# Kernel tuning notes

Hardware: AMD Instinct MI355X
Metric: run time of the kernel (lower is better)

The kernel has to match this reference:

```python
import jax, jax.numpy as jnp
import numpy as np

D_MODEL = 1024
N_HEADS = 16
D_HEAD = D_MODEL // N_HEADS

def setup_inputs() -> dict:
    key = jax.random.key(0)
    ks = jax.random.split(key, 5)
    B, T = 4, 2048
    s = 1.0 / np.sqrt(D_MODEL)
    return {
        "x": jax.random.normal(ks[0], (B, T, D_MODEL), dtype=jnp.float32),
        "qkv_w": jax.random.normal(ks[1], (3 * D_MODEL, D_MODEL), dtype=jnp.float32) * s,
        "qkv_b": jnp.zeros((3 * D_MODEL,), dtype=jnp.float32),
        "out_w": jax.random.normal(ks[2], (D_MODEL, D_MODEL), dtype=jnp.float32) * s,
        "out_b": jnp.zeros((D_MODEL,), dtype=jnp.float32),
    }

def reference(x, qkv_w, qkv_b, out_w, out_b):
    B, T, D = x.shape
    # fused QKV projection: [B,T,3D] -> [3,B,H,T,dh]
    qkv = (x @ qkv_w.T + qkv_b).reshape(B, T, 3, N_HEADS, D_HEAD)
    qkv = jnp.transpose(qkv, (2, 0, 3, 1, 4))
    q, k, v = qkv[0], qkv[1], qkv[2]
    scale = 1.0 / np.sqrt(D_HEAD).astype(np.float32)
    scores = jnp.einsum("bhqd,bhkd->bhqk", q, k) * scale
    attn = jax.nn.softmax(scores, axis=-1)
    ctx = jnp.einsum("bhqk,bhkd->bhqd", attn, v)  # [B,H,T,dh]
    ctx = jnp.transpose(ctx, (0, 2, 1, 3)).reshape(B, T, D)
    return ctx @ out_w.T + out_b
```

## Files before the change

### kernel.cpp

```cpp
#include <hip/hip_runtime.h>
#include <hip/hip_bf16.h>
#include <cstdint>
#include <cstddef>


#define SEQ 2048
#define DM 1024

typedef __attribute__((ext_vector_type(8))) short bf16x8;
typedef __attribute__((ext_vector_type(4))) short bf16x4;
typedef __attribute__((ext_vector_type(4))) float f32x4;

static __device__ __forceinline__ short f2bf(float f) {
  union { float f; uint32_t u; } v; v.f = f;
  uint32_t r = v.u + 0x7fffu + ((v.u >> 16) & 1u);
  return (short)(r >> 16);
}

typedef const __attribute__((address_space(1))) unsigned int* gas_ptr;
typedef __attribute__((address_space(3))) unsigned int* las_ptr;
static __device__ __forceinline__ void gl2lds16(const void* g, void* l) {
  __builtin_amdgcn_global_load_lds((gas_ptr)g, (las_ptr)l, 16, 0, 0);
}

static __device__ __forceinline__ unsigned permhi(float a_odd, float a_even) {
  union { float f; unsigned u; } x, y; x.f = a_odd; y.f = a_even;
  return __builtin_amdgcn_perm(x.u, y.u, 0x07060302u);
}
static __device__ __forceinline__ bf16x8 pack8t(const float* e) {
  union { bf16x8 v; unsigned u[4]; } r;
  r.u[0] = permhi(e[1], e[0]);
  r.u[1] = permhi(e[3], e[2]);
  r.u[2] = permhi(e[5], e[4]);
  r.u[3] = permhi(e[7], e[6]);
  return r.v;
}

static __device__ __forceinline__ int swz(int r) {
  return (r & 3) | (((r >> 3) & 1) << 2);
}

__global__ __launch_bounds__(256)
void cvt_bf16(const float* __restrict__ src, short* __restrict__ dst) {
  int i = blockIdx.x * 256 + threadIdx.x;
  float4 v = ((const float4*)src)[i];
  bf16x4 p = { f2bf(v.x), f2bf(v.y), f2bf(v.z), f2bf(v.w) };
  ((bf16x4*)dst)[i] = p;
}

__global__ __launch_bounds__(256, 2)
void qkv_gemm(const short* __restrict__ Xb, const short* __restrict__ Wb,
              const float* __restrict__ bias,
              short* __restrict__ Q, short* __restrict__ K,
              short* __restrict__ Vt) {
  __shared__ short As[2][128 * 64];
  __shared__ short Bs[2][128 * 64];
  const int tid  = threadIdx.x;
  const int m0   = blockIdx.x * 128;
  const int n0   = blockIdx.y * 128;
  const int lane = tid & 63;
  const int w    = tid >> 6;
  const int wm   = (w >> 1) * 64, wn = (w & 1) * 64;
  const int l15  = lane & 15, quad = lane >> 4;

  int g_row[4], g_col[4];
#pragma unroll
  for (int p = 0; p < 4; p++) {
    int r = p * 32 + w * 8 + (lane >> 3);
    g_row[p] = r;
    g_col[p] = ((lane & 7) ^ swz(r)) << 3;
  }
  int aoff[4][2], boff[4][2];
#pragma unroll
  for (int i = 0; i < 4; i++)
#pragma unroll
    for (int ks = 0; ks < 2; ks++) {
      int Ra = wm + i * 16 + l15;
      aoff[i][ks] = Ra * 128 + (((ks * 4 + quad) ^ swz(Ra)) << 4);
      int Rb = wn + i * 16 + l15;
      boff[i][ks] = Rb * 128 + (((ks * 4 + quad) ^ swz(Rb)) << 4);
    }

  f32x4 acc[4][4];
  for (int i = 0; i < 4; i++)
    for (int j = 0; j < 4; j++) acc[i][j] = (f32x4)0.0f;

#pragma unroll
  for (int p = 0; p < 4; p++) {
    gl2lds16(&Xb[(size_t)(m0 + g_row[p]) * DM + g_col[p]], &As[0][(p * 32 + w * 8) * 64]);
    gl2lds16(&Wb[(size_t)(n0 + g_row[p]) * DM + g_col[p]], &Bs[0][(p * 32 + w * 8) * 64]);
  }

  for (int t = 0; t < 16; t++) {
    const int cur = t & 1;
    if (t + 1 < 16) {
      const int kk = (t + 1) * 64;
#pragma unroll
      for (int p = 0; p < 4; p++) {
        gl2lds16(&Xb[(size_t)(m0 + g_row[p]) * DM + kk + g_col[p]], &As[cur ^ 1][(p * 32 + w * 8) * 64]);
        gl2lds16(&Wb[(size_t)(n0 + g_row[p]) * DM + kk + g_col[p]], &Bs[cur ^ 1][(p * 32 + w * 8) * 64]);
      }
      asm volatile("s_waitcnt vmcnt(8)" ::: "memory");
    } else {
      asm volatile("s_waitcnt vmcnt(0)" ::: "memory");
    }
    __builtin_amdgcn_s_barrier();
    __builtin_amdgcn_sched_barrier(0);

    const char* Ab = (const char*)&As[cur][0];
    const char* Bb = (const char*)&Bs[cur][0];
#pragma unroll
    for (int ks = 0; ks < 2; ks++) {
      bf16x8 af[4], bfr[4];
      for (int i = 0; i < 4; i++) af[i]  = *(const bf16x8*)(Ab + aoff[i][ks]);
      for (int j = 0; j < 4; j++) bfr[j] = *(const bf16x8*)(Bb + boff[j][ks]);
      for (int i = 0; i < 4; i++)
        for (int j = 0; j < 4; j++)
          acc[i][j] = __builtin_amdgcn_mfma_f32_16x16x32_bf16(af[i], bfr[j], acc[i][j], 0, 0, 0);
    }
    __builtin_amdgcn_sched_barrier(0);
    __builtin_amdgcn_s_barrier();
    __builtin_amdgcn_sched_barrier(0);
  }

  const float C1 = 0.18033688011112042f;
  const int qkv = n0 >> 10;
  for (int i = 0; i < 4; i++) {
    const int m = m0 + wm + i * 16 + quad * 4;
    const int bb = m >> 11, t = m & 2047;
    for (int j = 0; j < 4; j++) {
      const int f  = n0 + wn + j * 16 + l15;
      const int fi = f & 1023;
      const int h  = fi >> 6, d = fi & 63;
      const float bv = bias[f];
      if (qkv == 2) {
        bf16x4 pk = { f2bf(acc[i][j][0] + bv), f2bf(acc[i][j][1] + bv),
                      f2bf(acc[i][j][2] + bv), f2bf(acc[i][j][3] + bv) };
        *(bf16x4*)&Vt[((size_t)(bb * 16 + h) * 64 + d) * SEQ + t] = pk;
      } else {
        short* dst = (qkv == 0) ? Q : K;
        const float sc = (qkv == 0) ? C1 : 1.0f;
        size_t base = ((size_t)(bb * 16 + h) * SEQ + t) * 64 + d;
        for (int r = 0; r < 4; r++)
          dst[base + (size_t)r * 64] = f2bf((acc[i][j][r] + bv) * sc);
      }
    }
  }
}

__global__ __launch_bounds__(256, 4)
void attn(const short* __restrict__ Q, const short* __restrict__ K,
          const short* __restrict__ Vt, short* __restrict__ ctx) {
  __shared__ short Ks[2][64 * 64];
  __shared__ short Vs[2][64 * 64];
  const int tid  = threadIdx.x;
  const int w    = tid >> 6, lane = tid & 63;
  const int l15  = lane & 15, quad = lane >> 4;
  const int bh   = blockIdx.y;
  const int qr   = blockIdx.x * 128 + w * 32;
  const short* Kb = &K[(size_t)bh * SEQ * 64];
  const short* Vb = &Vt[(size_t)bh * 64 * SEQ];

  const int kperm = (l15 >> 2) * 8 + (l15 & 3);

  int dr[2], dc[2];
#pragma unroll
  for (int p = 0; p < 2; p++) {
    int ci = p * 256 + w * 64 + lane;
    dr[p] = ci >> 3;
    dc[p] = (ci & 7) ^ swz(ci >> 3);
  }
  const short* kp[2];
  const short* vp[2];
#pragma unroll
  for (int p = 0; p < 2; p++) {
    kp[p] = &Kb[(size_t)(64 + dr[p]) * 64 + dc[p] * 8];
    vp[p] = &Vb[(size_t)dr[p] * SEQ + 64 + dc[p] * 8];
  }

  int koff[2][2][2][2];
  int voff[2][4][2];
#pragma unroll
  for (int blk = 0; blk < 2; blk++)
#pragma unroll
    for (int tau = 0; tau < 2; tau++)
#pragma unroll
      for (int ks = 0; ks < 2; ks++) {
        int R = blk * 32 + kperm + tau * 4;
        int c = (ks * 4 + quad) ^ swz(R);
        int off = (R * 8 + c) * 16;
        koff[0][blk][tau][ks] = off;
        koff[1][blk][tau][ks] = off + 8192;
      }
#pragma unroll
  for (int dt = 0; dt < 4; dt++)
#pragma unroll
    for (int blk = 0; blk < 2; blk++) {
      int R = dt * 16 + l15;
      int c = (blk * 4 + quad) ^ swz(R);
      int off = (R * 8 + c) * 16;
      voff[0][dt][blk] = off;
      voff[1][dt][blk] = off + 8192;
    }
  const char* KsB = (const char*)&Ks[0][0];
  const char* VsB = (const char*)&Vs[0][0];

  bf16x8 qf[2][2];
#pragma unroll
  for (int mt = 0; mt < 2; mt++)
#pragma unroll
    for (int ks = 0; ks < 2; ks++)
      qf[mt][ks] = *(const bf16x8*)&Q[(size_t)bh * SEQ * 64 + (size_t)(qr + mt * 16 + l15) * 64 + ks * 32 + quad * 8];

  f32x4 O[2][4];
#pragma unroll
  for (int mt = 0; mt < 2; mt++)
    for (int dt = 0; dt < 4; dt++) O[mt][dt] = (f32x4)0.0f;
  f32x4 psA[2];
  psA[0] = (f32x4)0.0f; psA[1] = (f32x4)0.0f;
  const short one_bf = (short)0x3F80;
  const bf16x8 ones = { one_bf, one_bf, one_bf, one_bf, one_bf, one_bf, one_bf, one_bf };

#pragma unroll
  for (int p = 0; p < 2; p++) {
    gl2lds16(&Kb[(size_t)dr[p] * 64 + dc[p] * 8],  &Ks[0][(p * 256 + w * 64) * 8]);
    gl2lds16(&Vb[(size_t)dr[p] * SEQ + dc[p] * 8], &Vs[0][(p * 256 + w * 64) * 8]);
  }
  __syncthreads();

  for (int k0 = 0; k0 < SEQ; k0 += 128) {
#pragma unroll
    for (int half = 0; half < 2; half++) {
      const bool doPf = (half == 0) || (k0 + 128 < SEQ);
      if (doPf) {
#pragma unroll
        for (int p = 0; p < 2; p++) {
          gl2lds16(kp[p], &Ks[half ^ 1][(p * 256 + w * 64) * 8]);
          gl2lds16(vp[p], &Vs[half ^ 1][(p * 256 + w * 64) * 8]);
        }
      }
#pragma unroll
      for (int p = 0; p < 2; p++) { kp[p] += 64 * 64; vp[p] += 64; }

      bf16x8 kf[2][2][2];
#pragma unroll
      for (int blk = 0; blk < 2; blk++)
#pragma unroll
        for (int tau = 0; tau < 2; tau++)
#pragma unroll
          for (int ks = 0; ks < 2; ks++)
            kf[blk][tau][ks] = *(const bf16x8*)(KsB + koff[half][blk][tau][ks]);

      f32x4 S[2][2][2];
#pragma unroll
      for (int mt = 0; mt < 2; mt++)
#pragma unroll
        for (int blk = 0; blk < 2; blk++) {
          f32x4 S0 = (f32x4)0.0f, S1 = (f32x4)0.0f;
#pragma unroll
          for (int ks = 0; ks < 2; ks++) {
            S0 = __builtin_amdgcn_mfma_f32_16x16x32_bf16(kf[blk][0][ks], qf[mt][ks], S0, 0, 0, 0);
            S1 = __builtin_amdgcn_mfma_f32_16x16x32_bf16(kf[blk][1][ks], qf[mt][ks], S1, 0, 0, 0);
          }
          S[mt][blk][0] = S0; S[mt][blk][1] = S1;
        }

      bf16x8 vf[4][2];
#pragma unroll
      for (int dt = 0; dt < 4; dt++)
#pragma unroll
        for (int blk = 0; blk < 2; blk++)
          vf[dt][blk] = *(const bf16x8*)(VsB + voff[half][dt][blk]);

      bf16x8 pp[2][2];
#pragma unroll
      for (int mt = 0; mt < 2; mt++)
#pragma unroll
        for (int blk = 0; blk < 2; blk++) {
          float e[8];
#pragma unroll
          for (int r = 0; r < 4; r++) {
            e[r]     = exp2f(S[mt][blk][0][r]);
            e[4 + r] = exp2f(S[mt][blk][1][r]);
          }
          pp[mt][blk] = pack8t(e);
        }

#pragma unroll
      for (int blk = 0; blk < 2; blk++) {
#pragma unroll
        for (int dt = 0; dt < 4; dt++) {
          O[0][dt] = __builtin_amdgcn_mfma_f32_16x16x32_bf16(vf[dt][blk], pp[0][blk], O[0][dt], 0, 0, 0);
          O[1][dt] = __builtin_amdgcn_mfma_f32_16x16x32_bf16(vf[dt][blk], pp[1][blk], O[1][dt], 0, 0, 0);
        }
        psA[0] = __builtin_amdgcn_mfma_f32_16x16x32_bf16(ones, pp[0][blk], psA[0], 0, 0, 0);
        psA[1] = __builtin_amdgcn_mfma_f32_16x16x32_bf16(ones, pp[1][blk], psA[1], 0, 0, 0);
      }

      __syncthreads();
    }
  }

  const int bb = bh >> 4, h = bh & 15;
#pragma unroll
  for (int mt = 0; mt < 2; mt++) {
    float rinv = 1.0f / psA[mt][0];
    const int t = qr + mt * 16 + l15;
#pragma unroll
    for (int dt = 0; dt < 4; dt++) {
      bf16x4 ov = { f2bf(O[mt][dt][0] * rinv), f2bf(O[mt][dt][1] * rinv),
                    f2bf(O[mt][dt][2] * rinv), f2bf(O[mt][dt][3] * rinv) };
      *(bf16x4*)&ctx[(size_t)(bb * SEQ + t) * DM + h * 64 + dt * 16 + quad * 4] = ov;
    }
  }
}

__global__ __launch_bounds__(256, 2)
void out_gemm(const short* __restrict__ Cx, const short* __restrict__ Ob,
              const float* __restrict__ bias, float* __restrict__ Y) {
  __shared__ short As[2][128 * 64];
  __shared__ short Bs[2][128 * 64];
  const int tid  = threadIdx.x;
  const int m0   = blockIdx.x * 128;
  const int n0   = blockIdx.y * 128;
  const int lane = tid & 63;
  const int w    = tid >> 6;
  const int wm   = (w >> 1) * 64, wn = (w & 1) * 64;
  const int l15  = lane & 15, quad = lane >> 4;

  int g_row[4], g_col[4];
#pragma unroll
  for (int p = 0; p < 4; p++) {
    int r = p * 32 + w * 8 + (lane >> 3);
    g_row[p] = r;
    g_col[p] = ((lane & 7) ^ swz(r)) << 3;
  }
  int aoff[4][2], boff[4][2];
#pragma unroll
  for (int i = 0; i < 4; i++)
#pragma unroll
    for (int ks = 0; ks < 2; ks++) {
      int Ra = wm + i * 16 + l15;
      aoff[i][ks] = Ra * 128 + (((ks * 4 + quad) ^ swz(Ra)) << 4);
      int Rb = wn + i * 16 + l15;
      boff[i][ks] = Rb * 128 + (((ks * 4 + quad) ^ swz(Rb)) << 4);
    }

  f32x4 acc[4][4];
  for (int i = 0; i < 4; i++)
    for (int j = 0; j < 4; j++) acc[i][j] = (f32x4)0.0f;

#pragma unroll
  for (int p = 0; p < 4; p++) {
    gl2lds16(&Cx[(size_t)(m0 + g_row[p]) * DM + g_col[p]], &As[0][(p * 32 + w * 8) * 64]);
    gl2lds16(&Ob[(size_t)(n0 + g_row[p]) * DM + g_col[p]], &Bs[0][(p * 32 + w * 8) * 64]);
  }

  for (int t = 0; t < 16; t++) {
    const int cur = t & 1;
    if (t + 1 < 16) {
      const int kk = (t + 1) * 64;
#pragma unroll
      for (int p = 0; p < 4; p++) {
        gl2lds16(&Cx[(size_t)(m0 + g_row[p]) * DM + kk + g_col[p]], &As[cur ^ 1][(p * 32 + w * 8) * 64]);
        gl2lds16(&Ob[(size_t)(n0 + g_row[p]) * DM + kk + g_col[p]], &Bs[cur ^ 1][(p * 32 + w * 8) * 64]);
      }
      asm volatile("s_waitcnt vmcnt(8)" ::: "memory");
    } else {
      asm volatile("s_waitcnt vmcnt(0)" ::: "memory");
    }
    __builtin_amdgcn_s_barrier();
    __builtin_amdgcn_sched_barrier(0);

    const char* Ab = (const char*)&As[cur][0];
    const char* Bb = (const char*)&Bs[cur][0];
#pragma unroll
    for (int ks = 0; ks < 2; ks++) {
      bf16x8 af[4], bfr[4];
      for (int i = 0; i < 4; i++) af[i]  = *(const bf16x8*)(Ab + aoff[i][ks]);
      for (int j = 0; j < 4; j++) bfr[j] = *(const bf16x8*)(Bb + boff[j][ks]);
      for (int i = 0; i < 4; i++)
        for (int j = 0; j < 4; j++)
          acc[i][j] = __builtin_amdgcn_mfma_f32_16x16x32_bf16(af[i], bfr[j], acc[i][j], 0, 0, 0);
    }
    __builtin_amdgcn_sched_barrier(0);
    __builtin_amdgcn_s_barrier();
    __builtin_amdgcn_sched_barrier(0);
  }

  for (int i = 0; i < 4; i++) {
    const int m = m0 + wm + i * 16 + quad * 4;
    for (int j = 0; j < 4; j++) {
      const int n = n0 + wn + j * 16 + l15;
      const float bv = bias[n];
      for (int r = 0; r < 4; r++)
        Y[(size_t)(m + r) * DM + n] = acc[i][j][r] + bv;
    }
  }
}

extern "C" void kernel_launch(void* const* d_in, const int* in_sizes, int n_in,
                              void* d_out, int out_size, void* d_ws, size_t ws_size,
                              hipStream_t stream) {
  const float* x     = (const float*)d_in[0];
  const float* qkv_w = (const float*)d_in[1];
  const float* qkv_b = (const float*)d_in[2];
  const float* out_w = (const float*)d_in[3];
  const float* out_b = (const float*)d_in[4];
  float* out = (float*)d_out;

  const size_t NBH = (size_t)4 * 16 * SEQ * 64;
  short* Q   = (short*)d_ws;
  short* K   = Q + NBH;
  short* Vt  = K + NBH;
  short* ctx = Vt + NBH;
  short* Xb  = ctx;
  short* Ob  = Vt;
  short* Wb  = (short*)d_out;

  cvt_bf16<<<dim3(8192), 256, 0, stream>>>(x, Xb);
  cvt_bf16<<<dim3(3072), 256, 0, stream>>>(qkv_w, Wb);
  qkv_gemm<<<dim3(64, 24), 256, 0, stream>>>(Xb, Wb, qkv_b, Q, K, Vt);
  attn<<<dim3(SEQ / 128, 64), 256, 0, stream>>>(Q, K, Vt, ctx);
  cvt_bf16<<<dim3(1024), 256, 0, stream>>>(out_w, Ob);
  out_gemm<<<dim3(64, 8), 256, 0, stream>>>(ctx, Ob, out_b, out);
}
```

Before: 279.0 us.

## Enlarge QKV GEMM tile to 256x256 with 512 threads and fuse conversions

Grows the QKV projection GEMM block tile from 128x128 to 256x256 using 8 waves, each computing 128x64. This raises operand reuse from LDS and global memory. The main loop is restructured: it prefetches the next stage, hoists B fragments, wraps the MFMA block in s_setprio, and waits on vmcnt(0) before the barrier instead of a partial count. The two fp32-to-bf16 conversion launches for x and qkv_w are merged into one. The larger tile uses 128KB of LDS and many more accumulator registers, which lowers occupancy and leaves only 384 blocks.

```diff
diff --git a/kernel.cpp b/kernel.cpp
--- a/kernel.cpp
+++ b/kernel.cpp
@@ -48,48 +48,75 @@
   ((bf16x4*)dst)[i] = p;
 }
 
-__global__ __launch_bounds__(256, 2)
+__global__ __launch_bounds__(256)
+void cvt_bf16_2(const float* __restrict__ src1, short* __restrict__ dst1, int n1,
+                const float* __restrict__ src2, short* __restrict__ dst2) {
+  int b = blockIdx.x;
+  if (b < n1) {
+    int i = b * 256 + threadIdx.x;
+    float4 v = ((const float4*)src1)[i];
+    bf16x4 p = { f2bf(v.x), f2bf(v.y), f2bf(v.z), f2bf(v.w) };
+    ((bf16x4*)dst1)[i] = p;
+  } else {
+    int i = (b - n1) * 256 + threadIdx.x;
+    float4 v = ((const float4*)src2)[i];
+    bf16x4 p = { f2bf(v.x), f2bf(v.y), f2bf(v.z), f2bf(v.w) };
+    ((bf16x4*)dst2)[i] = p;
+  }
+}
+
+__global__ __launch_bounds__(512, 2)
 void qkv_gemm(const short* __restrict__ Xb, const short* __restrict__ Wb,
               const float* __restrict__ bias,
               short* __restrict__ Q, short* __restrict__ K,
               short* __restrict__ Vt) {
-  __shared__ short As[2][128 * 64];
-  __shared__ short Bs[2][128 * 64];
+  __shared__ short As[2][256 * 64];
+  __shared__ short Bs[2][256 * 64];
   const int tid  = threadIdx.x;
-  const int m0   = blockIdx.x * 128;
-  const int n0   = blockIdx.y * 128;
   const int lane = tid & 63;
   const int w    = tid >> 6;
-  const int wm   = (w >> 1) * 64, wn = (w & 1) * 64;
+  const int wr   = w >> 2, wc = w & 3;
   const int l15  = lane & 15, quad = lane >> 4;
-
-  int g_row[4], g_col[4];
+  const int m0   = blockIdx.x * 256;
+  const int n0   = blockIdx.y * 256;
+
+  int s_row[4], s_col[4];
 #pragma unroll
   for (int p = 0; p < 4; p++) {
-    int r = p * 32 + w * 8 + (lane >> 3);
-    g_row[p] = r;
-    g_col[p] = ((lane & 7) ^ swz(r)) << 3;
-  }
-  int aoff[4][2], boff[4][2];
-#pragma unroll
-  for (int i = 0; i < 4; i++)
+    int r = p * 64 + w * 8 + (lane >> 3);
+    s_row[p] = r;
+    s_col[p] = ((lane & 7) ^ swz(r)) << 3;
+  }
+  int aoff[8][2], boff[4][2];
+#pragma unroll
+  for (int mi = 0; mi < 8; mi++)
 #pragma unroll
     for (int ks = 0; ks < 2; ks++) {
-      int Ra = wm + i * 16 + l15;
-      aoff[i][ks] = Ra * 128 + (((ks * 4 + quad) ^ swz(Ra)) << 4);
-      int Rb = wn + i * 16 + l15;
-      boff[i][ks] = Rb * 128 + (((ks * 4 + quad) ^ swz(Rb)) << 4);
-    }
-
-  f32x4 acc[4][4];
-  for (int i = 0; i < 4; i++)
-    for (int j = 0; j < 4; j++) acc[i][j] = (f32x4)0.0f;
+      int R = wr * 128 + mi * 16 + l15;
+      aoff[mi][ks] = R * 128 + (((ks * 4 + quad) ^ swz(R)) << 4);
+    }
+#pragma unroll
+  for (int nj = 0; nj < 4; nj++)
+#pragma unroll
+    for (int ks = 0; ks < 2; ks++) {
+      int R = wc * 64 + nj * 16 + l15;
+      boff[nj][ks] = R * 128 + (((ks * 4 + quad) ^ swz(R)) << 4);
+    }
+
+  f32x4 acc[8][4];
+#pragma unroll
+  for (int mi = 0; mi < 8; mi++)
+#pragma unroll
+    for (int nj = 0; nj < 4; nj++) acc[mi][nj] = (f32x4)0.0f;
 
 #pragma unroll
   for (int p = 0; p < 4; p++) {
-    gl2lds16(&Xb[(size_t)(m0 + g_row[p]) * DM + g_col[p]], &As[0][(p * 32 + w * 8) * 64]);
-    gl2lds16(&Wb[(size_t)(n0 + g_row[p]) * DM + g_col[p]], &Bs[0][(p * 32 + w * 8) * 64]);
-  }
+    gl2lds16(&Xb[(size_t)(m0 + s_row[p]) * DM + s_col[p]], &As[0][(p * 64 + w * 8) * 64]);
+    gl2lds16(&Wb[(size_t)(n0 + s_row[p]) * DM + s_col[p]], &Bs[0][(p * 64 + w * 8) * 64]);
+  }
+  asm volatile("s_waitcnt vmcnt(0)" ::: "memory");
+  __builtin_amdgcn_s_barrier();
+  __builtin_amdgcn_sched_barrier(0);
 
   for (int t = 0; t < 16; t++) {
     const int cur = t & 1;
@@ -97,52 +124,58 @@
       const int kk = (t + 1) * 64;
 #pragma unroll
       for (int p = 0; p < 4; p++) {
-        gl2lds16(&Xb[(size_t)(m0 + g_row[p]) * DM + kk + g_col[p]], &As[cur ^ 1][(p * 32 + w * 8) * 64]);
-        gl2lds16(&Wb[(size_t)(n0 + g_row[p]) * DM + kk + g_col[p]], &Bs[cur ^ 1][(p * 32 + w * 8) * 64]);
-      }
-      asm volatile("s_waitcnt vmcnt(8)" ::: "memory");
-    } else {
-      asm volatile("s_waitcnt vmcnt(0)" ::: "memory");
-    }
+        gl2lds16(&Xb[(size_t)(m0 + s_row[p]) * DM + kk + s_col[p]], &As[cur ^ 1][(p * 64 + w * 8) * 64]);
+        gl2lds16(&Wb[(size_t)(n0 + s_row[p]) * DM + kk + s_col[p]], &Bs[cur ^ 1][(p * 64 + w * 8) * 64]);
+      }
+    }
+    const char* Ab = (const char*)&As[cur][0];
+    const char* Bb = (const char*)&Bs[cur][0];
+    bf16x8 bfr[4][2];
+#pragma unroll
+    for (int nj = 0; nj < 4; nj++)
+#pragma unroll
+      for (int ks = 0; ks < 2; ks++)
+        bfr[nj][ks] = *(const bf16x8*)(Bb + boff[nj][ks]);
+    __builtin_amdgcn_s_setprio(1);
+#pragma unroll
+    for (int mi = 0; mi < 8; mi++) {
+      bf16x8 af0 = *(const bf16x8*)(Ab + aoff[mi][0]);
+      bf16x8 af1 = *(const bf16x8*)(Ab + aoff[mi][1]);
+#pragma unroll
+      for (int nj = 0; nj < 4; nj++) {
+        acc[mi][nj] = __builtin_amdgcn_mfma_f32_16x16x32_bf16(af0, bfr[nj][0], acc[mi][nj], 0, 0, 0);
+        acc[mi][nj] = __builtin_amdgcn_mfma_f32_16x16x32_bf16(af1, bfr[nj][1], acc[mi][nj], 0, 0, 0);
+      }
+    }
+    __builtin_amdgcn_s_setprio(0);
+    __builtin_amdgcn_sched_barrier(0);
+    asm volatile("s_waitcnt vmcnt(0)" ::: "memory");
     __builtin_amdgcn_s_barrier();
     __builtin_amdgcn_sched_barrier(0);
-
-    const char* Ab = (const char*)&As[cur][0];
-    const char* Bb = (const char*)&Bs[cur][0];
-#pragma unroll
-    for (int ks = 0; ks < 2; ks++) {
-      bf16x8 af[4], bfr[4];
-      for (int i = 0; i < 4; i++) af[i]  = *(const bf16x8*)(Ab + aoff[i][ks]);
-      for (int j = 0; j < 4; j++) bfr[j] = *(const bf16x8*)(Bb + boff[j][ks]);
-      for (int i = 0; i < 4; i++)
-        for (int j = 0; j < 4; j++)
-          acc[i][j] = __builtin_amdgcn_mfma_f32_16x16x32_bf16(af[i], bfr[j], acc[i][j], 0, 0, 0);
-    }
-    __builtin_amdgcn_sched_barrier(0);
-    __builtin_amdgcn_s_barrier();
-    __builtin_amdgcn_sched_barrier(0);
   }
 
   const float C1 = 0.18033688011112042f;
   const int qkv = n0 >> 10;
-  for (int i = 0; i < 4; i++) {
-    const int m = m0 + wm + i * 16 + quad * 4;
+#pragma unroll
+  for (int mi = 0; mi < 8; mi++) {
+    const int m = m0 + wr * 128 + mi * 16 + quad * 4;
     const int bb = m >> 11, t = m & 2047;
-    for (int j = 0; j < 4; j++) {
-      const int f  = n0 + wn + j * 16 + l15;
+#pragma unroll
+    for (int nj = 0; nj < 4; nj++) {
+      const int f  = n0 + wc * 64 + nj * 16 + l15;
       const int fi = f & 1023;
       const int h  = fi >> 6, d = fi & 63;
       const float bv = bias[f];
       if (qkv == 2) {
-        bf16x4 pk = { f2bf(acc[i][j][0] + bv), f2bf(acc[i][j][1] + bv),
-                      f2bf(acc[i][j][2] + bv), f2bf(acc[i][j][3] + bv) };
+        bf16x4 pk = { f2bf(acc[mi][nj][0] + bv), f2bf(acc[mi][nj][1] + bv),
+                      f2bf(acc[mi][nj][2] + bv), f2bf(acc[mi][nj][3] + bv) };
         *(bf16x4*)&Vt[((size_t)(bb * 16 + h) * 64 + d) * SEQ + t] = pk;
       } else {
         short* dst = (qkv == 0) ? Q : K;
         const float sc = (qkv == 0) ? C1 : 1.0f;
         size_t base = ((size_t)(bb * 16 + h) * SEQ + t) * 64 + d;
         for (int r = 0; r < 4; r++)
-          dst[base + (size_t)r * 64] = f2bf((acc[i][j][r] + bv) * sc);
+          dst[base + (size_t)r * 64] = f2bf((acc[mi][nj][r] + bv) * sc);
       }
     }
   }
@@ -418,9 +451,8 @@
   short* Ob  = Vt;
   short* Wb  = (short*)d_out;
 
-  cvt_bf16<<<dim3(8192), 256, 0, stream>>>(x, Xb);
-  cvt_bf16<<<dim3(3072), 256, 0, stream>>>(qkv_w, Wb);
-  qkv_gemm<<<dim3(64, 24), 256, 0, stream>>>(Xb, Wb, qkv_b, Q, K, Vt);
+  cvt_bf16_2<<<dim3(8192 + 3072), 256, 0, stream>>>(x, Xb, 8192, qkv_w, Wb);
+  qkv_gemm<<<dim3(32, 12), 512, 0, stream>>>(Xb, Wb, qkv_b, Q, K, Vt);
   attn<<<dim3(SEQ / 128, 64), 256, 0, stream>>>(Q, K, Vt, ctx);
   cvt_bf16<<<dim3(1024), 256, 0, stream>>>(out_w, Ob);
   out_gemm<<<dim3(64, 8), 256, 0, stream>>>(ctx, Ob, out_b, out);
```

New measurement: 288.7 us. 1.03x slower.
